# Kernel optimization log

Hardware: AMD Instinct MI355X
Metric: run time of the kernel (lower is better)

Reference implementation:

```python
import jax, jax.numpy as jnp
import numpy as np

N, E = 10000, 100000   # nodes, edges
C = 64                 # sphere_channels
L2 = 9                 # (lmax+1)^2 with lmax=2
H, DH, DV = 8, 16, 16  # heads, alpha channels/head, value channels/head
EC = 64                # edge scalar channels
NRBF = 128             # radial basis size
ZMAX = 90              # max_num_elements


def setup_inputs() -> dict:
    key = jax.random.key(0)
    ks = jax.random.split(key, 12)
    inp = {}
    inp["node_embedding"] = jax.random.normal(ks[0], (N, L2, C), jnp.float32)
    inp["atomic_numbers"] = jax.random.randint(ks[1], (N,), 0, ZMAX)
    inp["edge_distance"] = jax.random.uniform(ks[2], (E,), jnp.float32)
    inp["edge_index"] = jax.random.randint(ks[3], (2, E), 0, N)
    # per-edge Wigner rotation into the edge-aligned SO(2) frame
    inp["wigner"] = jax.random.normal(ks[4], (E, L2, L2), jnp.float32) / np.sqrt(L2)
    # learned parameters
    inp["atom_emb"] = jax.random.normal(ks[5], (ZMAX, EC), jnp.float32) * 0.1
    inp["W_rbf"] = jax.random.normal(ks[6], (NRBF, EC), jnp.float32) / np.sqrt(NRBF)
    inp["W_gate"] = jax.random.normal(ks[7], (EC, H * DH), jnp.float32) / np.sqrt(EC)
    inp["W_msg"] = jax.random.normal(ks[8], (2 * C, H * DH), jnp.float32) / np.sqrt(2 * C)
    inp["alpha_vec"] = jax.random.normal(ks[9], (H, DH), jnp.float32) / np.sqrt(DH)
    inp["W_val"] = jax.random.normal(ks[10], (H * DH, H * DV), jnp.float32) / np.sqrt(H * DH)
    inp["W_out"] = jax.random.normal(ks[11], (H * DV, 1), jnp.float32) / np.sqrt(H * DV)
    return inp


def reference(node_embedding, atomic_numbers, edge_distance, edge_index, wigner,
              atom_emb, W_rbf, W_gate, W_msg, alpha_vec, W_val, W_out):
    src, dst = edge_index[0], edge_index[1]
    # --- edge scalar embedding: gaussian RBF of distance + endpoint atom embeddings ---
    centers = jnp.linspace(0.0, 1.0, NRBF, dtype=node_embedding.dtype)
    width = 1.0 / NRBF
    rbf = jnp.exp(-((edge_distance[:, None] - centers) ** 2) / (2.0 * width * width))  # [E, NRBF]
    edge_scalar = jax.nn.silu(rbf @ W_rbf + atom_emb[atomic_numbers[src]] + atom_emb[atomic_numbers[dst]])  # [E, EC]
    gate = jax.nn.silu(edge_scalar @ W_gate)  # [E, H*DH]
    # --- gather endpoint embeddings and rotate into edge frame (SO3 rotation) ---
    x_s = jnp.einsum('eij,ejc->eic', wigner, node_embedding[src])  # [E, L2, C]
    x_t = jnp.einsum('eij,ejc->eic', wigner, node_embedding[dst])  # [E, L2, C]
    msg = jnp.concatenate([x_s, x_t], axis=-1) @ W_msg            # [E, L2, H*DH]
    msg = msg * gate[:, None, :]
    # --- attention logits from the invariant (l=0) component ---
    a = msg[:, 0, :].reshape(E, H, DH)
    logits = jnp.einsum('ehd,hd->eh', jax.nn.leaky_relu(a, 0.2), alpha_vec)  # [E, H]
    # --- softmax over incoming edges of each destination node ---
    m = jax.ops.segment_max(logits, dst, num_segments=N)  # [N, H]
    ex = jnp.exp(logits - m[dst])
    den = jax.ops.segment_sum(ex, dst, num_segments=N)
    attn = ex / (den[dst] + 1e-9)  # [E, H]
    # --- attention-weighted values, rotate back, scatter-sum to nodes ---
    v = (msg @ W_val).reshape(E, L2, H, DV)
    v = v * attn[:, None, :, None]
    v = jnp.einsum('eji,ejhv->eihv', wigner, v).reshape(E, L2, H * DV)  # rotate back (R^T)
    node_out = jax.ops.segment_sum(v, dst, num_segments=N)  # [N, L2, H*DV]
    out = node_out @ W_out                                   # [N, L2, 1]
    forces = out[:, 1:4, 0]                                  # narrow(1,1,3).view(-1,3)
    return forces
```

## Files before the change

kernel.cpp:

```cpp
#include <hip/hip_runtime.h>
#include <hip/hip_bf16.h>

#define NN 10000
#define NE 100000

typedef __attribute__((ext_vector_type(8))) short short8v;
typedef __attribute__((ext_vector_type(4))) float float4v;

__device__ __forceinline__ float bcast(float v, int k) {
  return __int_as_float(__builtin_amdgcn_readlane(__float_as_int(v), k));
}
__device__ __forceinline__ unsigned int enc_f(float f) {
  unsigned int u = __float_as_uint(f);
  return (u & 0x80000000u) ? ~u : (u | 0x80000000u);
}
__device__ __forceinline__ float dec_f(unsigned int u) {
  return __uint_as_float((u & 0x80000000u) ? (u & 0x7fffffffu) : ~u);
}
__device__ __forceinline__ float silu_f(float x) {
  return x / (1.0f + __expf(-x));
}
__device__ __forceinline__ void f32_hilo(float x, short& h, short& l) {
  __hip_bfloat16 bh = __float2bfloat16(x);
  float r = x - __bfloat162float(bh);
  __hip_bfloat16 bl = __float2bfloat16(r);
  h = __builtin_bit_cast(short, bh);
  l = __builtin_bit_cast(short, bl);
}
#define MFMA16(a, b, c) __builtin_amdgcn_mfma_f32_16x16x32_bf16(a, b, c, 0, 0, 0)

__global__ void prep_kernel(const float* __restrict__ W_msg, const float* __restrict__ W_val,
                            const float* __restrict__ W_out, const float* __restrict__ W_rbf,
                            const float* __restrict__ W_gate,
                            float* __restrict__ Q, float* __restrict__ WmsgT,
                            short* __restrict__ Wp1h, short* __restrict__ Wp1l,
                            short* __restrict__ Wp2h, short* __restrict__ Wp2l,
                            short* __restrict__ Wp3h, short* __restrict__ Wp3l) {
  int i = blockIdx.x * blockDim.x + threadIdx.x;
  if (i < 1024) {
    int c = i >> 3, h = i & 7;
    float s = 0.0f;
#pragma unroll
    for (int dv = 0; dv < 16; ++dv)
      s += W_val[c * 128 + h * 16 + dv] * W_out[h * 16 + dv];
    Q[c * 8 + h] = s;
  }
  if (i < 16384) {
    int c = i >> 7, k = i & 127;
    WmsgT[c * 128 + k] = W_msg[k * 128 + c];
  }
  const float* W; short* ph; short* pl; int KF, Nw, local;
  if (i < 8192)       { W = W_rbf;  ph = Wp1h; pl = Wp1l; KF = 4; Nw = 64;  local = i; }
  else if (i < 16384) { W = W_gate; ph = Wp2h; pl = Wp2l; KF = 2; Nw = 128; local = i - 8192; }
  else                { W = W_msg;  ph = Wp3h; pl = Wp3l; KF = 4; Nw = 128; local = i - 16384; }
  int tile = local >> 9;
  int ln = (local >> 3) & 63;
  int j = local & 7;
  int nt = tile / KF, kf = tile % KF;
  int k = kf * 32 + 8 * (ln >> 4) + j;
  int n = nt * 16 + (ln & 15);
  float w = W[k * Nw + n];
  short h, lo;
  f32_hilo(w, h, lo);
  ph[local] = h;
  pl[local] = lo;
}

__global__ __launch_bounds__(256) void pass1_kernel(
    const float* __restrict__ nb, const int* __restrict__ zn,
    const float* __restrict__ dist, const int* __restrict__ ei,
    const float* __restrict__ wig, const float* __restrict__ aemb,
    const float* __restrict__ alpha,
    const short* __restrict__ Wp1h, const short* __restrict__ Wp1l,
    const short* __restrict__ Wp2h, const short* __restrict__ Wp2l,
    const short* __restrict__ Wp3h, const short* __restrict__ Wp3l,
    float* __restrict__ logits, unsigned int* __restrict__ m_enc,
    __hip_bfloat16* __restrict__ gate_ws) {
  __shared__ __attribute__((aligned(16))) float es_s[4][16][68];
  __shared__ __attribute__((aligned(16))) float xc_s[4][16][132];
  const int tid = threadIdx.x;
  const int lane = tid & 63;
  const int wid = tid >> 6;
  const int g = lane >> 4;
  const int col = lane & 15;
  const int e0 = (blockIdx.x * 4 + wid) * 16;

#pragma unroll 4
  for (int e = 0; e < 16; ++e) {
    int eu = e0 + e; if (eu >= NE) eu = NE - 1;
    int se = __builtin_amdgcn_readfirstlane(ei[eu]);
    int de = __builtin_amdgcn_readfirstlane(ei[NE + eu]);
    const float* __restrict__ pw = wig + (size_t)eu * 81;
    const float* __restrict__ ps = nb + (size_t)se * 576 + lane;
    const float* __restrict__ pt = nb + (size_t)de * 576 + lane;
    float xs = 0.0f, xt = 0.0f;
#pragma unroll
    for (int j = 0; j < 9; ++j) {
      float wj = pw[j];
      xs += wj * ps[j * 64];
      xt += wj * pt[j * 64];
    }
    xc_s[wid][e][lane] = xs;
    xc_s[wid][e][64 + lane] = xt;
  }

  int ecol = e0 + col; if (ecol >= NE) ecol = NE - 1;
  const float d = dist[ecol];
  short8v a1h[4], a1l[4];
#pragma unroll
  for (int kf = 0; kf < 4; ++kf) {
#pragma unroll
    for (int j = 0; j < 8; ++j) {
      int k = kf * 32 + 8 * g + j;
      float t = d - (float)k * (1.0f / 127.0f);
      float v = __expf(-8192.0f * t * t);
      short h, lo; f32_hilo(v, h, lo);
      a1h[kf][j] = h; a1l[kf][j] = lo;
    }
  }

  const float4v z4 = {0.0f, 0.0f, 0.0f, 0.0f};

  float4v acc1[4];
#pragma unroll
  for (int nt = 0; nt < 4; ++nt) {
    float4v a = z4;
#pragma unroll
    for (int kf = 0; kf < 4; ++kf) {
      short8v bh = *(const short8v*)(Wp1h + ((nt * 4 + kf) * 64 + lane) * 8);
      short8v bl = *(const short8v*)(Wp1l + ((nt * 4 + kf) * 64 + lane) * 8);
      a = MFMA16(a1h[kf], bh, a);
      a = MFMA16(a1h[kf], bl, a);
      a = MFMA16(a1l[kf], bh, a);
    }
    acc1[nt] = a;
  }

  int dn_r[4];
#pragma unroll
  for (int r = 0; r < 4; ++r) {
    int er = e0 + 4 * g + r;
    int erc = er < NE ? er : NE - 1;
    int sn = ei[erc];
    dn_r[r] = ei[NE + erc];
    int zs = zn[sn], zd = zn[dn_r[r]];
#pragma unroll
    for (int nt = 0; nt < 4; ++nt) {
      float b = aemb[zs * 64 + nt * 16 + col] + aemb[zd * 64 + nt * 16 + col];
      es_s[wid][4 * g + r][nt * 16 + col] = silu_f(acc1[nt][r] + b);
    }
  }
  __syncthreads();

  short8v a2h[2], a2l[2];
#pragma unroll
  for (int kf = 0; kf < 2; ++kf) {
    const float* p = &es_s[wid][col][kf * 32 + 8 * g];
    float4v v0 = *(const float4v*)p;
    float4v v1 = *(const float4v*)(p + 4);
#pragma unroll
    for (int j = 0; j < 4; ++j) {
      short h, lo;
      f32_hilo(v0[j], h, lo); a2h[kf][j] = h;     a2l[kf][j] = lo;
      f32_hilo(v1[j], h, lo); a2h[kf][4 + j] = h; a2l[kf][4 + j] = lo;
    }
  }

  float gate_r[8][4];
#pragma unroll
  for (int nt = 0; nt < 8; ++nt) {
    float4v a = z4;
#pragma unroll
    for (int kf = 0; kf < 2; ++kf) {
      short8v bh = *(const short8v*)(Wp2h + ((nt * 2 + kf) * 64 + lane) * 8);
      short8v bl = *(const short8v*)(Wp2l + ((nt * 2 + kf) * 64 + lane) * 8);
      a = MFMA16(a2h[kf], bh, a);
      a = MFMA16(a2h[kf], bl, a);
      a = MFMA16(a2l[kf], bh, a);
    }
#pragma unroll
    for (int r = 0; r < 4; ++r) {
      float gv = silu_f(a[r]);
      gate_r[nt][r] = gv;
      int er = e0 + 4 * g + r;
      if (er < NE)
        gate_ws[(size_t)er * 128 + nt * 16 + col] = __float2bfloat16(gv);
    }
  }

  short8v a3h[4], a3l[4];
#pragma unroll
  for (int kf = 0; kf < 4; ++kf) {
    const float* p = &xc_s[wid][col][kf * 32 + 8 * g];
    float4v v0 = *(const float4v*)p;
    float4v v1 = *(const float4v*)(p + 4);
#pragma unroll
    for (int j = 0; j < 4; ++j) {
      short h, lo;
      f32_hilo(v0[j], h, lo); a3h[kf][j] = h;     a3l[kf][j] = lo;
      f32_hilo(v1[j], h, lo); a3h[kf][4 + j] = h; a3l[kf][4 + j] = lo;
    }
  }

#pragma unroll
  for (int nt = 0; nt < 8; ++nt) {
    float4v a = z4;
#pragma unroll
    for (int kf = 0; kf < 4; ++kf) {
      short8v bh = *(const short8v*)(Wp3h + ((nt * 4 + kf) * 64 + lane) * 8);
      short8v bl = *(const short8v*)(Wp3l + ((nt * 4 + kf) * 64 + lane) * 8);
      a = MFMA16(a3h[kf], bh, a);
      a = MFMA16(a3h[kf], bl, a);
      a = MFMA16(a3l[kf], bh, a);
    }
    float al = alpha[nt * 16 + col];
#pragma unroll
    for (int r = 0; r < 4; ++r) {
      float v = a[r] * gate_r[nt][r];
      v = v > 0.0f ? v : 0.2f * v;
      v *= al;
#pragma unroll
      for (int off = 1; off < 16; off <<= 1) v += __shfl_xor(v, off);
      int er = e0 + 4 * g + r;
      if (col == 0 && er < NE) {
        logits[(size_t)er * 8 + nt] = v;
        atomicMax(&m_enc[dn_r[r] * 8 + nt], enc_f(v));
      }
    }
  }
}

__global__ void pass2_kernel(const float* __restrict__ logits,
                             const int* __restrict__ ei,
                             const unsigned int* __restrict__ m_enc,
                             float* __restrict__ den) {
  int i = blockIdx.x * blockDim.x + threadIdx.x;
  if (i >= NE * 8) return;
  int e = i >> 3, h = i & 7;
  int dn = ei[NE + e];
  float mm = dec_f(m_enc[dn * 8 + h]);
  atomicAdd(&den[dn * 8 + h], __expf(logits[i] - mm));
}

__global__ __launch_bounds__(256) void pass3_kernel(
    const float* __restrict__ nb, const int* __restrict__ ei,
    const float* __restrict__ wig, const float* __restrict__ logits,
    const unsigned int* __restrict__ m_enc, const float* __restrict__ den,
    const __hip_bfloat16* __restrict__ gate_ws, const float* __restrict__ Q,
    const float* __restrict__ WmsgT, float* __restrict__ out) {
  const int lane = threadIdx.x & 63;
  const int wid = threadIdx.x >> 6;
  const int e0 = (blockIdx.x * 4 + wid) * 4;

  int src[4], dst[4];
#pragma unroll
  for (int e = 0; e < 4; ++e) {
    src[e] = ei[e0 + e];
    dst[e] = ei[NE + e0 + e];
  }

  float attn_v = 0.0f;
  if (lane < 32) {
    int e = lane >> 3, h = lane & 7;
    int dn = ei[NE + e0 + e];
    float l = logits[(size_t)(e0 + e) * 8 + h];
    float mm = dec_f(m_enc[dn * 8 + h]);
    float dv = den[dn * 8 + h];
    attn_v = __expf(l - mm) / (dv + 1e-9f);
  }

  float g0[4], g1[4];
#pragma unroll
  for (int e = 0; e < 4; ++e) {
    g0[e] = __bfloat162float(gate_ws[(size_t)(e0 + e) * 128 + lane]);
    g1[e] = __bfloat162float(gate_ws[(size_t)(e0 + e) * 128 + 64 + lane]);
  }

  float wv0[4] = {0, 0, 0, 0}, wv1[4] = {0, 0, 0, 0};
#pragma unroll
  for (int h = 0; h < 8; ++h) {
    float q0 = Q[lane * 8 + h];
    float q1 = Q[(lane + 64) * 8 + h];
#pragma unroll
    for (int e = 0; e < 4; ++e) {
      float a = bcast(attn_v, e * 8 + h);
      wv0[e] += q0 * a;
      wv1[e] += q1 * a;
    }
  }
  float u0[4], u1[4];
#pragma unroll
  for (int e = 0; e < 4; ++e) {
    u0[e] = g0[e] * wv0[e];
    u1[e] = g1[e] * wv1[e];
  }

  float t0[4] = {0, 0, 0, 0}, t1[4] = {0, 0, 0, 0};
#pragma unroll 8
  for (int c = 0; c < 64; ++c) {
    float w00 = WmsgT[c * 128 + lane];
    float w01 = WmsgT[c * 128 + 64 + lane];
    float w10 = WmsgT[(c + 64) * 128 + lane];
    float w11 = WmsgT[(c + 64) * 128 + 64 + lane];
#pragma unroll
    for (int e = 0; e < 4; ++e) {
      float a0 = bcast(u0[e], c);
      float a1 = bcast(u1[e], c);
      t0[e] += a0 * w00 + a1 * w10;
      t1[e] += a0 * w01 + a1 * w11;
    }
  }

#pragma unroll
  for (int e = 0; e < 4; ++e) {
    const float* ps = nb + (size_t)src[e] * 576 + lane;
    const float* pt = nb + (size_t)dst[e] * 576 + lane;
    float dj[9];
#pragma unroll
    for (int j = 0; j < 9; ++j) {
      float p = ps[j * 64] * t0[e] + pt[j * 64] * t1[e];
#pragma unroll
      for (int off = 32; off >= 1; off >>= 1) p += __shfl_xor(p, off);
      dj[j] = p;
    }
    const float* we = wig + (size_t)(e0 + e) * 81;
    float s_j = 0.0f;
    if (lane < 9) {
#pragma unroll
      for (int jp = 0; jp < 9; ++jp) s_j += we[lane * 9 + jp] * dj[jp];
    }
    if (lane >= 1 && lane <= 3) {
      float f = 0.0f;
#pragma unroll
      for (int j = 0; j < 9; ++j) f += bcast(s_j, j) * we[j * 9 + lane];
      atomicAdd(&out[dst[e] * 3 + (lane - 1)], f);
    }
  }
}

extern "C" void kernel_launch(void* const* d_in, const int* in_sizes, int n_in,
                              void* d_out, int out_size, void* d_ws, size_t ws_size,
                              hipStream_t stream) {
  const float* nb = (const float*)d_in[0];
  const int* zn = (const int*)d_in[1];
  const float* dist = (const float*)d_in[2];
  const int* ei = (const int*)d_in[3];
  const float* wig = (const float*)d_in[4];
  const float* aemb = (const float*)d_in[5];
  const float* W_rbf = (const float*)d_in[6];
  const float* W_gate = (const float*)d_in[7];
  const float* W_msg = (const float*)d_in[8];
  const float* alpha = (const float*)d_in[9];
  const float* W_val = (const float*)d_in[10];
  const float* W_out = (const float*)d_in[11];
  float* out = (float*)d_out;

  char* p = (char*)d_ws;
  float* Q = (float*)p;                   p += 1024 * 4;
  float* WmsgT = (float*)p;               p += 16384 * 4;
  unsigned int* m_enc = (unsigned int*)p; p += (size_t)NN * 8 * 4;
  float* den = (float*)p;                 p += (size_t)NN * 8 * 4;
  float* logits = (float*)p;              p += (size_t)NE * 8 * 4;
  __hip_bfloat16* gate_ws = (__hip_bfloat16*)p; p += (size_t)NE * 128 * 2;
  short* Wp1h = (short*)p; p += 8192 * 2;
  short* Wp1l = (short*)p; p += 8192 * 2;
  short* Wp2h = (short*)p; p += 8192 * 2;
  short* Wp2l = (short*)p; p += 8192 * 2;
  short* Wp3h = (short*)p; p += 16384 * 2;
  short* Wp3l = (short*)p; p += 16384 * 2;

  hipMemsetAsync(d_out, 0, (size_t)NN * 3 * 4, stream);
  hipMemsetAsync(m_enc, 0, (size_t)NN * 8 * 4, stream);
  hipMemsetAsync(den, 0, (size_t)NN * 8 * 4, stream);

  prep_kernel<<<128, 256, 0, stream>>>(W_msg, W_val, W_out, W_rbf, W_gate, Q, WmsgT,
                                       Wp1h, Wp1l, Wp2h, Wp2l, Wp3h, Wp3l);
  pass1_kernel<<<(NE + 63) / 64, 256, 0, stream>>>(nb, zn, dist, ei, wig, aemb, alpha,
                                                   Wp1h, Wp1l, Wp2h, Wp2l, Wp3h, Wp3l,
                                                   logits, m_enc, gate_ws);
  pass2_kernel<<<(NE * 8) / 256, 256, 0, stream>>>(logits, ei, m_enc, den);
  pass3_kernel<<<NE / 16, 256, 0, stream>>>(nb, ei, wig, logits, m_enc, den,
                                            gate_ws, Q, WmsgT, out);
}
```

Before: 356.2 us.

## Move pass3 W_msg-transpose product onto bf16x3 MFMA with 16-edge wave tiles

Pass3 now handles 16 edges per wave instead of 4. It stages the attention-scaled gate vectors in shared memory and computes their product with W_msg transposed using split-bf16 (hi/lo, three-term) 16x16x32 MFMA, in place of a scalar FMA loop with readlane broadcasts. The prep kernel packs a transposed W_msg into MFMA fragment layout and no longer writes the fp32 transpose. The final node-embedding dot products use float4 loads across 16-lane groups with shorter shuffle reductions. This is meant to cut VALU and broadcast cost and raise reuse of the weight loads, at the price of more shared memory, more registers and a small precision change from the bf16x3 emulation.

```diff
diff --git a/kernel.cpp b/kernel.cpp
--- a/kernel.cpp
+++ b/kernel.cpp
@@ -32,10 +32,11 @@
 __global__ void prep_kernel(const float* __restrict__ W_msg, const float* __restrict__ W_val,
                             const float* __restrict__ W_out, const float* __restrict__ W_rbf,
                             const float* __restrict__ W_gate,
-                            float* __restrict__ Q, float* __restrict__ WmsgT,
+                            float* __restrict__ Q,
                             short* __restrict__ Wp1h, short* __restrict__ Wp1l,
                             short* __restrict__ Wp2h, short* __restrict__ Wp2l,
-                            short* __restrict__ Wp3h, short* __restrict__ Wp3l) {
+                            short* __restrict__ Wp3h, short* __restrict__ Wp3l,
+                            short* __restrict__ Wp4h, short* __restrict__ Wp4l) {
   int i = blockIdx.x * blockDim.x + threadIdx.x;
   if (i < 1024) {
     int c = i >> 3, h = i & 7;
@@ -45,21 +46,18 @@
       s += W_val[c * 128 + h * 16 + dv] * W_out[h * 16 + dv];
     Q[c * 8 + h] = s;
   }
-  if (i < 16384) {
-    int c = i >> 7, k = i & 127;
-    WmsgT[c * 128 + k] = W_msg[k * 128 + c];
-  }
-  const float* W; short* ph; short* pl; int KF, Nw, local;
+  const float* W; short* ph; short* pl; int KF, Nw, local; bool tr = false;
   if (i < 8192)       { W = W_rbf;  ph = Wp1h; pl = Wp1l; KF = 4; Nw = 64;  local = i; }
   else if (i < 16384) { W = W_gate; ph = Wp2h; pl = Wp2l; KF = 2; Nw = 128; local = i - 8192; }
-  else                { W = W_msg;  ph = Wp3h; pl = Wp3l; KF = 4; Nw = 128; local = i - 16384; }
+  else if (i < 32768) { W = W_msg;  ph = Wp3h; pl = Wp3l; KF = 4; Nw = 128; local = i - 16384; }
+  else                { W = W_msg;  ph = Wp4h; pl = Wp4l; KF = 4; Nw = 128; local = i - 32768; tr = true; }
   int tile = local >> 9;
   int ln = (local >> 3) & 63;
   int j = local & 7;
   int nt = tile / KF, kf = tile % KF;
   int k = kf * 32 + 8 * (ln >> 4) + j;
   int n = nt * 16 + (ln & 15);
-  float w = W[k * Nw + n];
+  float w = tr ? W[n * 128 + k] : W[k * Nw + n];
   short h, lo;
   f32_hilo(w, h, lo);
   ph[local] = h;
@@ -247,94 +245,123 @@
     const float* __restrict__ wig, const float* __restrict__ logits,
     const unsigned int* __restrict__ m_enc, const float* __restrict__ den,
     const __hip_bfloat16* __restrict__ gate_ws, const float* __restrict__ Q,
-    const float* __restrict__ WmsgT, float* __restrict__ out) {
-  const int lane = threadIdx.x & 63;
-  const int wid = threadIdx.x >> 6;
-  const int e0 = (blockIdx.x * 4 + wid) * 4;
-
-  int src[4], dst[4];
-#pragma unroll
-  for (int e = 0; e < 4; ++e) {
-    src[e] = ei[e0 + e];
-    dst[e] = ei[NE + e0 + e];
-  }
-
-  float attn_v = 0.0f;
-  if (lane < 32) {
-    int e = lane >> 3, h = lane & 7;
-    int dn = ei[NE + e0 + e];
-    float l = logits[(size_t)(e0 + e) * 8 + h];
+    const short* __restrict__ Wp4h, const short* __restrict__ Wp4l,
+    float* __restrict__ out) {
+  __shared__ __attribute__((aligned(16))) float attn_s[4][16][8];
+  __shared__ __attribute__((aligned(16))) float x_s[4][16][132];
+  const int tid = threadIdx.x;
+  const int lane = tid & 63;
+  const int wid = tid >> 6;
+  const int g = lane >> 4;
+  const int col = lane & 15;
+  const int e0 = (blockIdx.x * 4 + wid) * 16;
+
+#pragma unroll
+  for (int half = 0; half < 2; ++half) {
+    int i = half * 64 + lane;
+    int e = i >> 3, h = i & 7;
+    int ec = e0 + e; if (ec >= NE) ec = NE - 1;
+    int dn = ei[NE + ec];
+    float l = logits[(size_t)ec * 8 + h];
     float mm = dec_f(m_enc[dn * 8 + h]);
     float dv = den[dn * 8 + h];
-    attn_v = __expf(l - mm) / (dv + 1e-9f);
-  }
-
-  float g0[4], g1[4];
-#pragma unroll
-  for (int e = 0; e < 4; ++e) {
-    g0[e] = __bfloat162float(gate_ws[(size_t)(e0 + e) * 128 + lane]);
-    g1[e] = __bfloat162float(gate_ws[(size_t)(e0 + e) * 128 + 64 + lane]);
-  }
-
-  float wv0[4] = {0, 0, 0, 0}, wv1[4] = {0, 0, 0, 0};
+    attn_s[wid][e][h] = __expf(l - mm) / (dv + 1e-9f);
+  }
+
+  float q0[8], q1[8];
 #pragma unroll
   for (int h = 0; h < 8; ++h) {
-    float q0 = Q[lane * 8 + h];
-    float q1 = Q[(lane + 64) * 8 + h];
-#pragma unroll
-    for (int e = 0; e < 4; ++e) {
-      float a = bcast(attn_v, e * 8 + h);
-      wv0[e] += q0 * a;
-      wv1[e] += q1 * a;
-    }
-  }
-  float u0[4], u1[4];
-#pragma unroll
-  for (int e = 0; e < 4; ++e) {
-    u0[e] = g0[e] * wv0[e];
-    u1[e] = g1[e] * wv1[e];
-  }
-
-  float t0[4] = {0, 0, 0, 0}, t1[4] = {0, 0, 0, 0};
-#pragma unroll 8
-  for (int c = 0; c < 64; ++c) {
-    float w00 = WmsgT[c * 128 + lane];
-    float w01 = WmsgT[c * 128 + 64 + lane];
-    float w10 = WmsgT[(c + 64) * 128 + lane];
-    float w11 = WmsgT[(c + 64) * 128 + 64 + lane];
-#pragma unroll
-    for (int e = 0; e < 4; ++e) {
-      float a0 = bcast(u0[e], c);
-      float a1 = bcast(u1[e], c);
-      t0[e] += a0 * w00 + a1 * w10;
-      t1[e] += a0 * w01 + a1 * w11;
-    }
-  }
-
-#pragma unroll
-  for (int e = 0; e < 4; ++e) {
-    const float* ps = nb + (size_t)src[e] * 576 + lane;
-    const float* pt = nb + (size_t)dst[e] * 576 + lane;
+    q0[h] = Q[lane * 8 + h];
+    q1[h] = Q[(lane + 64) * 8 + h];
+  }
+#pragma unroll 4
+  for (int e = 0; e < 16; ++e) {
+    int ec = e0 + e; if (ec >= NE) ec = NE - 1;
+    float4v a0 = *(const float4v*)&attn_s[wid][e][0];
+    float4v a1 = *(const float4v*)&attn_s[wid][e][4];
+    float wv0 = 0.0f, wv1 = 0.0f;
+#pragma unroll
+    for (int h = 0; h < 4; ++h) {
+      wv0 += q0[h] * a0[h] + q0[4 + h] * a1[h];
+      wv1 += q1[h] * a0[h] + q1[4 + h] * a1[h];
+    }
+    float gg0 = __bfloat162float(gate_ws[(size_t)ec * 128 + lane]);
+    float gg1 = __bfloat162float(gate_ws[(size_t)ec * 128 + 64 + lane]);
+    x_s[wid][e][lane] = gg0 * wv0;
+    x_s[wid][e][64 + lane] = gg1 * wv1;
+  }
+
+  short8v ah[4], al[4];
+#pragma unroll
+  for (int kf = 0; kf < 4; ++kf) {
+    const float* p = &x_s[wid][col][kf * 32 + 8 * g];
+    float4v v0 = *(const float4v*)p;
+    float4v v1 = *(const float4v*)(p + 4);
+#pragma unroll
+    for (int j = 0; j < 4; ++j) {
+      short h, lo;
+      f32_hilo(v0[j], h, lo); ah[kf][j] = h;     al[kf][j] = lo;
+      f32_hilo(v1[j], h, lo); ah[kf][4 + j] = h; al[kf][4 + j] = lo;
+    }
+  }
+  const float4v z4 = {0.0f, 0.0f, 0.0f, 0.0f};
+  float4v acc[8];
+#pragma unroll
+  for (int nt = 0; nt < 8; ++nt) {
+    float4v a = z4;
+#pragma unroll
+    for (int kf = 0; kf < 4; ++kf) {
+      short8v bh = *(const short8v*)(Wp4h + ((nt * 4 + kf) * 64 + lane) * 8);
+      short8v bl = *(const short8v*)(Wp4l + ((nt * 4 + kf) * 64 + lane) * 8);
+      a = MFMA16(ah[kf], bh, a);
+      a = MFMA16(ah[kf], bl, a);
+      a = MFMA16(al[kf], bh, a);
+    }
+    acc[nt] = a;
+  }
+#pragma unroll
+  for (int nt = 0; nt < 8; ++nt)
+#pragma unroll
+    for (int r = 0; r < 4; ++r)
+      x_s[wid][4 * g + r][nt * 16 + col] = acc[nt][r];
+
+  const int cg = col * 4;
+#pragma unroll
+  for (int it = 0; it < 4; ++it) {
+    int e = it * 4 + g;
+    int eu = e0 + e;
+    bool valid = eu < NE;
+    int ec = valid ? eu : NE - 1;
+    int se = ei[ec], de = ei[NE + ec];
+    float4v t0 = *(const float4v*)&x_s[wid][e][cg];
+    float4v t1 = *(const float4v*)&x_s[wid][e][64 + cg];
+    const float* ps = nb + (size_t)se * 576 + cg;
+    const float* pt = nb + (size_t)de * 576 + cg;
     float dj[9];
 #pragma unroll
     for (int j = 0; j < 9; ++j) {
-      float p = ps[j * 64] * t0[e] + pt[j * 64] * t1[e];
-#pragma unroll
-      for (int off = 32; off >= 1; off >>= 1) p += __shfl_xor(p, off);
-      dj[j] = p;
-    }
-    const float* we = wig + (size_t)(e0 + e) * 81;
-    float s_j = 0.0f;
-    if (lane < 9) {
-#pragma unroll
-      for (int jp = 0; jp < 9; ++jp) s_j += we[lane * 9 + jp] * dj[jp];
-    }
-    if (lane >= 1 && lane <= 3) {
-      float f = 0.0f;
-#pragma unroll
-      for (int j = 0; j < 9; ++j) f += bcast(s_j, j) * we[j * 9 + lane];
-      atomicAdd(&out[dst[e] * 3 + (lane - 1)], f);
-    }
+      float4v a = *(const float4v*)(ps + j * 64);
+      float4v b = *(const float4v*)(pt + j * 64);
+      dj[j] = a[0] * t0[0] + a[1] * t0[1] + a[2] * t0[2] + a[3] * t0[3] +
+              b[0] * t1[0] + b[1] * t1[1] + b[2] * t1[2] + b[3] * t1[3];
+    }
+#pragma unroll
+    for (int j = 0; j < 9; ++j)
+#pragma unroll
+      for (int off = 1; off < 16; off <<= 1) dj[j] += __shfl_xor(dj[j], off);
+
+    const float* we = wig + (size_t)ec * 81;
+    int ls = col < 9 ? col : 8;
+    float s_l = 0.0f;
+#pragma unroll
+    for (int jp = 0; jp < 9; ++jp) s_l += we[ls * 9 + jp] * dj[jp];
+    int lc = (col >= 1 && col <= 3) ? col : 1;
+    float f = 0.0f;
+#pragma unroll
+    for (int j = 0; j < 9; ++j)
+      f += __shfl(s_l, (lane & 48) + j) * we[j * 9 + lc];
+    if (col >= 1 && col <= 3 && valid)
+      atomicAdd(&out[de * 3 + (col - 1)], f);
   }
 }
 
@@ -357,7 +384,6 @@
 
   char* p = (char*)d_ws;
   float* Q = (float*)p;                   p += 1024 * 4;
-  float* WmsgT = (float*)p;               p += 16384 * 4;
   unsigned int* m_enc = (unsigned int*)p; p += (size_t)NN * 8 * 4;
   float* den = (float*)p;                 p += (size_t)NN * 8 * 4;
   float* logits = (float*)p;              p += (size_t)NE * 8 * 4;
@@ -368,17 +394,19 @@
   short* Wp2l = (short*)p; p += 8192 * 2;
   short* Wp3h = (short*)p; p += 16384 * 2;
   short* Wp3l = (short*)p; p += 16384 * 2;
+  short* Wp4h = (short*)p; p += 16384 * 2;
+  short* Wp4l = (short*)p; p += 16384 * 2;
 
   hipMemsetAsync(d_out, 0, (size_t)NN * 3 * 4, stream);
   hipMemsetAsync(m_enc, 0, (size_t)NN * 8 * 4, stream);
   hipMemsetAsync(den, 0, (size_t)NN * 8 * 4, stream);
 
-  prep_kernel<<<128, 256, 0, stream>>>(W_msg, W_val, W_out, W_rbf, W_gate, Q, WmsgT,
-                                       Wp1h, Wp1l, Wp2h, Wp2l, Wp3h, Wp3l);
+  prep_kernel<<<192, 256, 0, stream>>>(W_msg, W_val, W_out, W_rbf, W_gate, Q,
+                                       Wp1h, Wp1l, Wp2h, Wp2l, Wp3h, Wp3l, Wp4h, Wp4l);
   pass1_kernel<<<(NE + 63) / 64, 256, 0, stream>>>(nb, zn, dist, ei, wig, aemb, alpha,
                                                    Wp1h, Wp1l, Wp2h, Wp2l, Wp3h, Wp3l,
                                                    logits, m_enc, gate_ws);
-  pass2_kernel<<<(NE * 8) / 256, 256, 0, stream>>>(logits, ei, m_enc, den);
-  pass3_kernel<<<NE / 16, 256, 0, stream>>>(nb, ei, wig, logits, m_enc, den,
-                                            gate_ws, Q, WmsgT, out);
-}
+  pass2_kernel<<<(NE * 8 + 255) / 256, 256, 0, stream>>>(logits, ei, m_enc, den);
+  pass3_kernel<<<(NE + 63) / 64, 256, 0, stream>>>(nb, ei, wig, logits, m_enc, den,
+                                                   gate_ws, Q, Wp4h, Wp4l, out);
+}
```

Result: faster. 325.2 us (-8.7%).
